# Optimization experiments

Measured on AMD Instinct MI355X. Metric: run time of the kernel, lower is better.

The kernel has to match this reference:

```python
import jax, jax.numpy as jnp
import numpy as np

MAX_LEN = 128
VOCAB = 32000
SENTINEL = 2**30  # larger than any valid token id; pushes masked slots to the end after sort


def setup_inputs() -> dict:
    key = jax.random.key(0)
    k1, k2, k3, k4 = jax.random.split(key, 4)
    B, L = 262144, MAX_LEN
    input_ids = jax.random.randint(k1, (B, L), 0, VOCAB, dtype=jnp.int32)
    attention_mask = jax.random.randint(k2, (B, L), 0, 2, dtype=jnp.int32)
    # MLP params: Linear(3,32) -> ReLU -> Linear(32,32) -> ReLU
    W1 = jax.random.normal(k3, (3, 32), dtype=jnp.float32) * (1.0 / np.sqrt(3.0))
    b1 = jnp.zeros((32,), dtype=jnp.float32)
    W2 = jax.random.normal(k4, (32, 32), dtype=jnp.float32) * (1.0 / np.sqrt(32.0))
    b2 = jnp.zeros((32,), dtype=jnp.float32)
    return {"input_ids": input_ids, "attention_mask": attention_mask,
            "W1": W1, "b1": b1, "W2": W2, "b2": b2}


def _symbolic_feats(input_ids, attention_mask):
    # Batched replacement of the per-row torch.unique loop:
    # sort masked tokens per row, count boundaries between distinct values.
    mask = attention_mask.astype(bool)
    seq_len = jnp.sum(mask, axis=1)  # [B]
    ids_m = jnp.where(mask, input_ids, SENTINEL)  # masked-out slots -> sentinel
    s = jnp.sort(ids_m, axis=1)  # valid tokens first (ids < SENTINEL)
    valid = s < SENTINEL
    first = jnp.ones((s.shape[0], 1), dtype=bool)
    new_val = jnp.concatenate([first, s[:, 1:] != s[:, :-1]], axis=1)
    uniq = jnp.sum(valid & new_val, axis=1)  # [B] unique count among valid tokens
    seq_f = seq_len.astype(jnp.float32)
    uniq_f = uniq.astype(jnp.float32)
    uniq_ratio = jnp.where(seq_len > 0, uniq_f / jnp.maximum(seq_f, 1.0), 0.0)
    feats = jnp.stack([seq_f / MAX_LEN, uniq_f / MAX_LEN, uniq_ratio], axis=1)  # [B,3]
    return feats


def reference(input_ids, attention_mask, W1, b1, W2, b2):
    feats = _symbolic_feats(input_ids, attention_mask)  # [B,3]
    h = jax.nn.relu(feats @ W1 + b1)
    out = jax.nn.relu(h @ W2 + b2)
    return out
```

## Files before the change

### kernel.cpp

```cpp
#include <hip/hip_runtime.h>

#define ROW_LEN 128
#define NPAIR (129 * 129)

__global__ __launch_bounds__(256) void mlp_table_kernel(
    const float* __restrict__ W1, const float* __restrict__ b1,
    const float* __restrict__ W2, const float* __restrict__ b2,
    float* __restrict__ table)
{
    const int tid = blockIdx.x * 256 + threadIdx.x;
    if (tid >= NPAIR * 32) return;
    const int p = tid >> 5;
    const int j = tid & 31;
    const int seq  = p / 129;
    const int uniq = p % 129;
    const float f0 = (float)seq  * (1.0f / 128.0f);
    const float f1 = (float)uniq * (1.0f / 128.0f);
    const float f2 = (seq > 0) ? ((float)uniq / (float)seq) : 0.0f;

    float acc = b2[j];
    #pragma unroll
    for (int jj = 0; jj < 32; ++jj) {
        float h = b1[jj];
        h = fmaf(f0, W1[jj],      h);
        h = fmaf(f1, W1[32 + jj], h);
        h = fmaf(f2, W1[64 + jj], h);
        h = fmaxf(h, 0.0f);
        acc = fmaf(h, W2[jj * 32 + j], acc);
    }
    table[tid] = fmaxf(acc, 0.0f);
}

__device__ __forceinline__ int pass_row(unsigned* mybm, const int4& id,
                                        const int4& mk, bool act)
{
    int s = 0, u = 0;
    #pragma unroll
    for (int j = 0; j < 4; ++j) {
        const int t = (j == 0) ? id.x : (j == 1) ? id.y : (j == 2) ? id.z : id.w;
        const int m = (j == 0) ? mk.x : (j == 1) ? mk.y : (j == 2) ? mk.z : mk.w;
        const bool v = act && (m != 0);
        int nw = 0;
        if (v) {
            const unsigned tt = (unsigned)t, bit = 1u << (tt & 31u);
            nw = ((atomicOr(&mybm[tt >> 5], bit) & bit) == 0u);
        }
        s += __popcll(__ballot(v));
        u += __popcll(__ballot(nw != 0));
    }
    return s * 129 + u;
}

__global__ __launch_bounds__(256, 8) void rows_kernel(
    const int* __restrict__ ids, const int* __restrict__ amask,
    const float* __restrict__ table, float* __restrict__ out, int B)
{
    __shared__ unsigned bm[4][1024];
    const int wave = threadIdx.x >> 6;
    const int lane = threadIdx.x & 63;
    unsigned* mybm = bm[wave];

    const long rowA = ((long)blockIdx.x * 4 + wave) * 2;
    if (rowA >= B) return;
    const long rowL = rowA + (lane >> 5);

    const int4* ids4 = (const int4*)ids;
    const int4* mk4v = (const int4*)amask;
    int4 id = make_int4(0, 0, 0, 0);
    int4 mk = make_int4(0, 0, 0, 0);
    if (rowL < B) {
        const long v = rowA * 32 + lane;
        id = ids4[v];
        mk = mk4v[v];
    }

    uint4* z = (uint4*)mybm;
    #pragma unroll
    for (int i = 0; i < 4; ++i) z[lane + i * 64] = make_uint4(0u, 0u, 0u, 0u);

    const int pA = pass_row(mybm, id, mk, lane < 32);

    #pragma unroll
    for (int i = 0; i < 4; ++i) z[lane + i * 64] = make_uint4(0u, 0u, 0u, 0u);

    const int pB = pass_row(mybm, id, mk, lane >= 32);

    if (rowL < B) {
        const int p = (lane < 32) ? pA : pB;
        out[rowA * 32 + lane] = table[p * 32 + (lane & 31)];
    }
}

extern "C" void kernel_launch(void* const* d_in, const int* in_sizes, int n_in,
                              void* d_out, int out_size, void* d_ws, size_t ws_size,
                              hipStream_t stream) {
    const int*   ids   = (const int*)d_in[0];
    const int*   amask = (const int*)d_in[1];
    const float* W1    = (const float*)d_in[2];
    const float* b1    = (const float*)d_in[3];
    const float* W2    = (const float*)d_in[4];
    const float* b2    = (const float*)d_in[5];
    float* out   = (float*)d_out;
    float* table = (float*)d_ws;

    const int B = in_sizes[0] / ROW_LEN;

    const int tblThreads = NPAIR * 32;
    mlp_table_kernel<<<(tblThreads + 255) / 256, 256, 0, stream>>>(W1, b1, W2, b2, table);

    const long pairs = ((long)B + 1) / 2;
    const int blocks = (int)((pairs + 3) / 4);
    rows_kernel<<<blocks, 256, 0, stream>>>(ids, amask, table, out, B);
}
```

Measured before the change: 287.7 us.

## Process both rows in one pass with interleaved per-row bitmap bits

Replaces the two sequential per-row bitmap passes with a single pass in which each 32-bit bitmap word holds 16 token slots for each of the two rows, interleaved by a row bit. This halves the atomicOr rounds and ballots and removes the second bitmap clear. In exchange the per-wave bitmap doubles to 8 KB, raising shared memory per block to 32 KB, and the occupancy hint drops from 8 to 5 blocks per CU.

```diff
diff --git a/kernel.cpp b/kernel.cpp
--- a/kernel.cpp
+++ b/kernel.cpp
@@ -31,31 +31,11 @@
     table[tid] = fmaxf(acc, 0.0f);
 }
 
-__device__ __forceinline__ int pass_row(unsigned* mybm, const int4& id,
-                                        const int4& mk, bool act)
-{
-    int s = 0, u = 0;
-    #pragma unroll
-    for (int j = 0; j < 4; ++j) {
-        const int t = (j == 0) ? id.x : (j == 1) ? id.y : (j == 2) ? id.z : id.w;
-        const int m = (j == 0) ? mk.x : (j == 1) ? mk.y : (j == 2) ? mk.z : mk.w;
-        const bool v = act && (m != 0);
-        int nw = 0;
-        if (v) {
-            const unsigned tt = (unsigned)t, bit = 1u << (tt & 31u);
-            nw = ((atomicOr(&mybm[tt >> 5], bit) & bit) == 0u);
-        }
-        s += __popcll(__ballot(v));
-        u += __popcll(__ballot(nw != 0));
-    }
-    return s * 129 + u;
-}
-
-__global__ __launch_bounds__(256, 8) void rows_kernel(
+__global__ __launch_bounds__(256, 5) void rows_kernel(
     const int* __restrict__ ids, const int* __restrict__ amask,
     const float* __restrict__ table, float* __restrict__ out, int B)
 {
-    __shared__ unsigned bm[4][1024];
+    __shared__ unsigned bm[4][2048];
     const int wave = threadIdx.x >> 6;
     const int lane = threadIdx.x & 63;
     unsigned* mybm = bm[wave];
@@ -76,14 +56,31 @@
 
     uint4* z = (uint4*)mybm;
     #pragma unroll
-    for (int i = 0; i < 4; ++i) z[lane + i * 64] = make_uint4(0u, 0u, 0u, 0u);
+    for (int i = 0; i < 8; ++i) z[lane + i * 64] = make_uint4(0u, 0u, 0u, 0u);
 
-    const int pA = pass_row(mybm, id, mk, lane < 32);
-
+    const unsigned rowbit = (lane >= 32) ? 1u : 0u;
+    int seqA = 0, seqB = 0, uniqA = 0, uniqB = 0;
     #pragma unroll
-    for (int i = 0; i < 4; ++i) z[lane + i * 64] = make_uint4(0u, 0u, 0u, 0u);
-
-    const int pB = pass_row(mybm, id, mk, lane >= 32);
+    for (int j = 0; j < 4; ++j) {
+        const int t = (j == 0) ? id.x : (j == 1) ? id.y : (j == 2) ? id.z : id.w;
+        const int m = (j == 0) ? mk.x : (j == 1) ? mk.y : (j == 2) ? mk.z : mk.w;
+        const bool v = (m != 0);
+        int nw = 0;
+        if (v) {
+            const unsigned tt  = (unsigned)t;
+            const unsigned bit = ((tt & 15u) << 1) | rowbit;
+            const unsigned msk = 1u << bit;
+            nw = ((atomicOr(&mybm[tt >> 4], msk) & msk) == 0u);
+        }
+        const unsigned long long vb = __ballot(v);
+        const unsigned long long nb = __ballot(nw != 0);
+        seqA  += __popc((unsigned)vb);
+        seqB  += __popc((unsigned)(vb >> 32));
+        uniqA += __popc((unsigned)nb);
+        uniqB += __popc((unsigned)(nb >> 32));
+    }
+    const int pA = seqA * 129 + uniqA;
+    const int pB = seqB * 129 + uniqB;
 
     if (rowL < B) {
         const int p = (lane < 32) ? pA : pB;
```

After: 283.2 us. Within noise of the previous version (-1.6%).
